# Kernel tuning notes

Hardware: AMD Instinct MI355X
Metric: run time of the kernel (lower is better)

## Reference

```python
import jax, jax.numpy as jnp
import numpy as np
import math

B, L, DM, DI, DS, DR, K, NL = 1, 1024, 768, 1536, 16, 48, 4, 2
DT_MIN, DT_MAX = 0.001, 0.1


def rmsnorm(x, w, eps=1e-5):
    return x * jax.lax.rsqrt(jnp.mean(x * x, axis=-1, keepdims=True) + eps) * w


def causal_dwconv(x, w, b):
    # x: [B,L,C], w: [C,1,K]. torch Conv1d(padding=K-1)[..., :L] == left-pad K-1 causal conv.
    y = jax.lax.conv_general_dilated(
        x.transpose(0, 2, 1), w, (1,), [(K - 1, 0)],
        dimension_numbers=('NCH', 'OIH', 'NCH'), feature_group_count=DI)
    return y.transpose(0, 2, 1) + b


def selective_scan(x, delta, A, Bm, Cm, D):
    # x, delta: [B,L,DI]; A: [DI,DS]; Bm, Cm: [B,L,DS]; D: [DI]
    dA = jnp.exp(delta[..., None] * A)               # [B,L,DI,DS]
    BX = (delta * x)[..., None] * Bm[:, :, None, :]  # [B,L,DI,DS]

    def comb(c1, c2):
        a1, b1 = c1
        a2, b2 = c2
        return (a1 * a2, a2 * b1 + b2)

    _, hs = jax.lax.associative_scan(comb, (dA, BX), axis=1)  # h_t = dA_t*h_{t-1} + BX_t
    return jnp.einsum('bldn,bln->bld', hs, Cm) + D * x


def ssm(x, xproj_w, dt_w, dt_b, A_log, D):
    dbc = jnp.einsum('bld,ed->ble', x, xproj_w)            # [B,L,DR+2*DS]
    dlt, Bm, Cm = jnp.split(dbc, [DR, DR + DS], axis=-1)
    delta = jax.nn.softplus(jnp.einsum('blr,dr->bld', dlt, dt_w) + dt_b)
    return selective_scan(x, delta, -jnp.exp(A_log), Bm, Cm, D)


def mamba_block(x, p):
    xz = jnp.einsum('bld,ed->ble', x, p['in_w'])           # [B,L,2*DI]
    xin, z = jnp.split(xz, 2, axis=-1)
    xf = jax.nn.silu(causal_dwconv(xin, p['cf_w'], p['cf_b']))
    xb = jax.nn.silu(causal_dwconv(xin[:, ::-1, :], p['cb_w'], p['cb_b']))
    yf = ssm(xf, p['xf_w'], p['dtf_w'], p['dtf_b'], p['Af'], p['Df'])
    yb = ssm(xb, p['xb_w'], p['dtb_w'], p['dtb_b'], p['Ab'], p['Db'])  # NOT flipped back (faithful)
    y = jnp.einsum('ble,de->bld', jnp.concatenate([yf, yb], axis=-1), p['pro_w']) + p['pro_b']
    # tokenizer: scores over L, softmax along L, mix values; dropout = identity (eval)
    att = jax.nn.softmax(jnp.einsum('bld,td->btl', y, p['wA']), axis=-1)  # [B,T=L,L]
    vv = jnp.einsum('bld,de->ble', y, p['wV'])
    y = jnp.einsum('btl,ble->bte', att, vv)
    return jnp.einsum('bld,od->blo', y * jax.nn.silu(z), p['out_w'])


def reference(x, norm_w, in_proj_w, conv_f_w, conv_f_b, conv_b_w, conv_b_b,
              xproj_f_w, xproj_b_w, dt_f_w, dt_f_b, dt_b_w, dt_b_b,
              A_log_f, D_f, A_log_b, D_b, out_w, token_wA, token_wV, pro_w, pro_b):
    for i in range(NL):
        p = dict(in_w=in_proj_w[i], cf_w=conv_f_w[i], cf_b=conv_f_b[i],
                 cb_w=conv_b_w[i], cb_b=conv_b_b[i], xf_w=xproj_f_w[i],
                 xb_w=xproj_b_w[i], dtf_w=dt_f_w[i], dtf_b=dt_f_b[i],
                 dtb_w=dt_b_w[i], dtb_b=dt_b_b[i], Af=A_log_f[i], Df=D_f[i],
                 Ab=A_log_b[i], Db=D_b[i], out_w=out_w[i], wA=token_wA[i],
                 wV=token_wV[i], pro_w=pro_w[i], pro_b=pro_b[i])
        x = x + mamba_block(rmsnorm(x, norm_w[i]), p)
    return x


def setup_inputs():
    key = jax.random.key(0)
    ks = jax.random.split(key, 16)
    rn = lambda k, sh, s=0.02: jax.random.normal(k, sh, jnp.float32) * s
    A_log = jnp.broadcast_to(jnp.log(jnp.arange(1, DS + 1, dtype=jnp.float32)), (NL, DI, DS))
    dt = jnp.exp(jax.random.uniform(ks[0], (NL, DI)) * (math.log(DT_MAX) - math.log(DT_MIN)) + math.log(DT_MIN))
    inv_dt = dt + jnp.log(-jnp.expm1(-dt))  # softplus^-1(dt)
    dt_std = DR ** -0.5
    kaiming = (2.0 / DI) ** 0.5
    return {
        'x': jax.random.normal(ks[1], (B, L, DM), jnp.float32),
        'norm_w': jnp.ones((NL, DM), jnp.float32),
        'in_proj_w': rn(ks[2], (NL, 2 * DI, DM)),
        'conv_f_w': rn(ks[3], (NL, DI, 1, K), 0.3),
        'conv_f_b': jnp.zeros((NL, DI), jnp.float32),
        'conv_b_w': rn(ks[4], (NL, DI, 1, K), 0.3),
        'conv_b_b': jnp.zeros((NL, DI), jnp.float32),
        'xproj_f_w': rn(ks[5], (NL, DR + 2 * DS, DI)),
        'xproj_b_w': rn(ks[6], (NL, DR + 2 * DS, DI)),
        'dt_f_w': jax.random.uniform(ks[7], (NL, DI, DR), jnp.float32, -dt_std, dt_std),
        'dt_f_b': inv_dt,
        'dt_b_w': jax.random.uniform(ks[8], (NL, DI, DR), jnp.float32, -dt_std, dt_std),
        'dt_b_b': inv_dt,
        'A_log_f': A_log,
        'D_f': jnp.ones((NL, DI), jnp.float32),
        'A_log_b': A_log,
        'D_b': jnp.ones((NL, DI), jnp.float32),
        'out_w': rn(ks[9], (NL, DM, DI)),
        'token_wA': rn(ks[10], (NL, L, DI), kaiming),
        'token_wV': rn(ks[11], (NL, DI, DI), kaiming),
        'pro_w': rn(ks[12], (NL, DI, 2 * DI)),
        'pro_b': jnp.zeros((NL, DI), jnp.float32),
    }
```

## Files before the change

### kernel.cpp

```cpp
#include <hip/hip_runtime.h>
#include <hip/hip_bf16.h>
#include <math.h>
#include <stdint.h>

#define LSEQ 1024
#define DMODEL 768
#define DINNER 1536
#define DSTATE 16
#define DRANK 48
#define KCONV 4
#define NLAYER 2
#define DBC 80
#define NQ 4
#define QL (LSEQ / NQ)
#define QCH (QL / 16)

typedef unsigned short u16;
typedef __attribute__((ext_vector_type(8))) __bf16 bf16x8;
typedef __attribute__((ext_vector_type(4))) float f32x4;
typedef __attribute__((ext_vector_type(4))) unsigned short us4;

__device__ __forceinline__ u16 f2bf(float f) {
  union { float f; unsigned u; } v; v.f = f;
  unsigned r = v.u + 0x7fffu + ((v.u >> 16) & 1u);
  return (u16)(r >> 16);
}
__device__ __forceinline__ float bf2f(u16 u) {
  union { unsigned u; float f; } v; v.u = ((unsigned)u) << 16;
  return v.f;
}

__device__ __forceinline__ void gload16(const void* g, void* l) {
  auto gp = reinterpret_cast<const __attribute__((address_space(1))) uint32_t*>(
      reinterpret_cast<uintptr_t>(g));
  auto lp = reinterpret_cast<__attribute__((address_space(3))) uint32_t*>(
      reinterpret_cast<uintptr_t>(l));
  __builtin_amdgcn_global_load_lds(gp, lp, 16, 0, 0);
}

#define CV0 589824
#define CV1 (CV0 + 1179648)
#define CV2 (CV1 + 393216)
#define CV3 (CV2 + 294912)
__global__ __launch_bounds__(256) void cvt4_k(
    const float* __restrict__ i0, u16* __restrict__ o0,
    const float* __restrict__ i1, u16* __restrict__ o1,
    const float* __restrict__ i2, u16* __restrict__ o2,
    const float* __restrict__ i3, u16* __restrict__ o3) {
  int i = blockIdx.x * 256 + threadIdx.x;
  const float* in; u16* out; int off;
  if (i < CV0)      { in = i0; out = o0; off = i; }
  else if (i < CV1) { in = i1; out = o1; off = i - CV0; }
  else if (i < CV2) { in = i2; out = o2; off = i - CV1; }
  else              { in = i3; out = o3; off = i - CV2; }
  float4 v = ((const float4*)in)[off];
  us4 o; o[0] = f2bf(v.x); o[1] = f2bf(v.y); o[2] = f2bf(v.z); o[3] = f2bf(v.w);
  ((us4*)out)[off] = o;
}

__global__ __launch_bounds__(256) void transcvt_k(const float* __restrict__ in,
                                                  u16* __restrict__ out,
                                                  int R, int C) {
  __shared__ float t[32][33];
  int c0 = blockIdx.x * 32, r0 = blockIdx.y * 32;
  int tx = threadIdx.x & 31, ty = threadIdx.x >> 5;
  for (int i = ty; i < 32; i += 8) t[i][tx] = in[(size_t)(r0 + i) * C + c0 + tx];
  __syncthreads();
  for (int i = ty; i < 32; i += 8)
    out[(size_t)(c0 + i) * R + r0 + tx] = f2bf(t[tx][i]);
}

__global__ __launch_bounds__(256) void transpose16_k(const u16* __restrict__ in,
                                                     u16* __restrict__ out,
                                                     int R, int C) {
  __shared__ u16 t[32][34];
  int c0 = blockIdx.x * 32, r0 = blockIdx.y * 32;
  int tx = threadIdx.x & 31, ty = threadIdx.x >> 5;
  for (int i = ty; i < 32; i += 8) t[i][tx] = in[(size_t)(r0 + i) * C + c0 + tx];
  __syncthreads();
  for (int i = ty; i < 32; i += 8)
    out[(size_t)(c0 + i) * R + r0 + tx] = t[tx][i];
}

__global__ __launch_bounds__(256) void rmsnorm_k(const float* __restrict__ x,
                                                 const float* __restrict__ w,
                                                 u16* __restrict__ xn) {
  int row = blockIdx.x;
  int tid = threadIdx.x;
  const float* xr = x + (size_t)row * DMODEL;
  float ss = 0.f;
  for (int j = tid; j < DMODEL; j += 256) { float v = xr[j]; ss += v * v; }
  __shared__ float red[256];
  red[tid] = ss; __syncthreads();
  for (int s = 128; s > 0; s >>= 1) { if (tid < s) red[tid] += red[tid + s]; __syncthreads(); }
  float scale = rsqrtf(red[0] / (float)DMODEL + 1e-5f);
  u16* outr = xn + (size_t)row * DMODEL;
  for (int j = tid; j < DMODEL; j += 256) outr[j] = f2bf(xr[j] * scale * w[j]);
}

template<int EPI>
__global__ __launch_bounds__(256) void mgemm_k(
    const u16* __restrict__ A, int lda,
    const u16* __restrict__ B, int ldb,
    void* __restrict__ Cv, int ldc, int K,
    const float* __restrict__ bias,
    const float* __restrict__ resid, int ldr)
{
  __shared__ u16 As[2][64 * 64];
  __shared__ u16 Bs[2][64 * 64];
  const int tid = threadIdx.x;
  const int lane = tid & 63;
  const int w = tid >> 6;

  const int nbx = gridDim.x;
  int bid = blockIdx.y * nbx + blockIdx.x;
  const int nwg = nbx * gridDim.y;
  bid = (bid & 7) * (nwg >> 3) + (bid >> 3);
  const int bm = (bid / nbx) * 64;
  const int bn = (bid % nbx) * 64;

  const int srow = lane >> 3;
  const int scs = (lane & 7) ^ srow;
  const int gA = 2 * w;
  const u16* Asrc0 = A + (size_t)(bm + gA * 8 + srow) * lda + scs * 8;
  const u16* Asrc1 = Asrc0 + (size_t)8 * lda;
  const u16* Bsrc0 = B + (size_t)(bn + gA * 8 + srow) * ldb + scs * 8;
  const u16* Bsrc1 = Bsrc0 + (size_t)8 * ldb;
  const int d0 = gA * 512;
  const int d1 = d0 + 512;

  const int fr = lane & 15;
  const int fs = lane >> 4;
  const int wm = (w >> 1) * 32;
  const int wn = (w & 1) * 32;
  int aoff[2][2], boff[2][2];
#pragma unroll
  for (int i = 0; i < 2; i++)
#pragma unroll
    for (int h = 0; h < 2; h++) {
      const int g = h * 4 + fs;
      aoff[i][h] = (wm + i * 16 + fr) * 64 + (g ^ (fr & 7)) * 8;
      boff[i][h] = (wn + i * 16 + fr) * 64 + (g ^ (fr & 7)) * 8;
    }

  f32x4 acc[2][2];
#pragma unroll
  for (int i = 0; i < 2; i++)
#pragma unroll
    for (int j = 0; j < 2; j++) acc[i][j] = (f32x4){0.f, 0.f, 0.f, 0.f};

#define STAGE(buf, k0) do { \
    gload16(Asrc0 + (k0), &As[buf][d0]); \
    gload16(Asrc1 + (k0), &As[buf][d1]); \
    gload16(Bsrc0 + (k0), &Bs[buf][d0]); \
    gload16(Bsrc1 + (k0), &Bs[buf][d1]); \
  } while (0)

  const int nk = K >> 6;
  STAGE(0, 0);

  for (int t = 0; t < nk; t++) {
    const int buf = t & 1;
    __syncthreads();
    if (t + 1 < nk) STAGE(buf ^ 1, (t + 1) << 6);
    const u16* As_ = As[buf];
    const u16* Bs_ = Bs[buf];
#pragma unroll
    for (int h = 0; h < 2; h++) {
      bf16x8 a0 = *reinterpret_cast<const bf16x8*>(As_ + aoff[0][h]);
      bf16x8 a1 = *reinterpret_cast<const bf16x8*>(As_ + aoff[1][h]);
      bf16x8 b0 = *reinterpret_cast<const bf16x8*>(Bs_ + boff[0][h]);
      bf16x8 b1 = *reinterpret_cast<const bf16x8*>(Bs_ + boff[1][h]);
      acc[0][0] = __builtin_amdgcn_mfma_f32_16x16x32_bf16(a0, b0, acc[0][0], 0, 0, 0);
      acc[0][1] = __builtin_amdgcn_mfma_f32_16x16x32_bf16(a0, b1, acc[0][1], 0, 0, 0);
      acc[1][0] = __builtin_amdgcn_mfma_f32_16x16x32_bf16(a1, b0, acc[1][0], 0, 0, 0);
      acc[1][1] = __builtin_amdgcn_mfma_f32_16x16x32_bf16(a1, b1, acc[1][1], 0, 0, 0);
    }
  }
#undef STAGE

#pragma unroll
  for (int i = 0; i < 2; i++) {
#pragma unroll
    for (int j = 0; j < 2; j++) {
      const int col = bn + wn + j * 16 + fr;
      const int row0 = bm + wm + i * 16 + fs * 4;
      float bv = (EPI & 1) ? bias[col] : 0.f;
#pragma unroll
      for (int r = 0; r < 4; r++) {
        float v = acc[i][j][r] + bv;
        if (EPI & 4) v += resid[(size_t)(row0 + r) * ldr + col];
        if (EPI & 16) {
          float z = resid[(size_t)(row0 + r) * ldr + col];
          v *= z / (1.f + __expf(-z));
        }
        if (EPI & 8) ((u16*)Cv)[(size_t)(row0 + r) * ldc + col] = f2bf(v);
        else         ((float*)Cv)[(size_t)(row0 + r) * ldc + col] = v;
      }
    }
  }
}

__global__ __launch_bounds__(256) void svgemm_k(
    const u16* __restrict__ wA, const u16* __restrict__ ypro,
    const u16* __restrict__ wVT,
    float* __restrict__ Smat, u16* __restrict__ vv)
{
  __shared__ u16 As[2][64 * 64];
  __shared__ u16 Bs[2][64 * 64];
  const int tid = threadIdx.x;
  const int lane = tid & 63;
  const int w = tid >> 6;

  int bid = blockIdx.x;
  bid = (bid & 7) * 80 + (bid >> 3);
  const bool is_s = bid < 256;
  const u16* A;
  const u16* B;
  int bm, bn;
  if (is_s) { A = wA;   B = ypro; bm = (bid >> 4) * 64;         bn = (bid & 15) * 64; }
  else      { A = ypro; B = wVT;  bm = ((bid - 256) / 24) * 64; bn = ((bid - 256) % 24) * 64; }

  const int srow = lane >> 3;
  const int scs = (lane & 7) ^ srow;
  const int gA = 2 * w;
  const u16* Asrc0 = A + (size_t)(bm + gA * 8 + srow) * DINNER + scs * 8;
  const u16* Asrc1 = Asrc0 + (size_t)8 * DINNER;
  const u16* Bsrc0 = B + (size_t)(bn + gA * 8 + srow) * DINNER + scs * 8;
  const u16* Bsrc1 = Bsrc0 + (size_t)8 * DINNER;
  const int d0 = gA * 512;
  const int d1 = d0 + 512;

  const int fr = lane & 15;
  const int fs = lane >> 4;
  const int wm = (w >> 1) * 32;
  const int wn = (w & 1) * 32;
  int aoff[2][2], boff[2][2];
#pragma unroll
  for (int i = 0; i < 2; i++)
#pragma unroll
    for (int h = 0; h < 2; h++) {
      const int g = h * 4 + fs;
      aoff[i][h] = (wm + i * 16 + fr) * 64 + (g ^ (fr & 7)) * 8;
      boff[i][h] = (wn + i * 16 + fr) * 64 + (g ^ (fr & 7)) * 8;
    }

  f32x4 acc[2][2];
#pragma unroll
  for (int i = 0; i < 2; i++)
#pragma unroll
    for (int j = 0; j < 2; j++) acc[i][j] = (f32x4){0.f, 0.f, 0.f, 0.f};

#define STAGE(buf, k0) do { \
    gload16(Asrc0 + (k0), &As[buf][d0]); \
    gload16(Asrc1 + (k0), &As[buf][d1]); \
    gload16(Bsrc0 + (k0), &Bs[buf][d0]); \
    gload16(Bsrc1 + (k0), &Bs[buf][d1]); \
  } while (0)

  STAGE(0, 0);
  for (int t = 0; t < DINNER / 64; t++) {
    const int buf = t & 1;
    __syncthreads();
    if (t + 1 < DINNER / 64) STAGE(buf ^ 1, (t + 1) << 6);
    const u16* As_ = As[buf];
    const u16* Bs_ = Bs[buf];
#pragma unroll
    for (int h = 0; h < 2; h++) {
      bf16x8 a0 = *reinterpret_cast<const bf16x8*>(As_ + aoff[0][h]);
      bf16x8 a1 = *reinterpret_cast<const bf16x8*>(As_ + aoff[1][h]);
      bf16x8 b0 = *reinterpret_cast<const bf16x8*>(Bs_ + boff[0][h]);
      bf16x8 b1 = *reinterpret_cast<const bf16x8*>(Bs_ + boff[1][h]);
      acc[0][0] = __builtin_amdgcn_mfma_f32_16x16x32_bf16(a0, b0, acc[0][0], 0, 0, 0);
      acc[0][1] = __builtin_amdgcn_mfma_f32_16x16x32_bf16(a0, b1, acc[0][1], 0, 0, 0);
      acc[1][0] = __builtin_amdgcn_mfma_f32_16x16x32_bf16(a1, b0, acc[1][0], 0, 0, 0);
      acc[1][1] = __builtin_amdgcn_mfma_f32_16x16x32_bf16(a1, b1, acc[1][1], 0, 0, 0);
    }
  }
#undef STAGE

#pragma unroll
  for (int i = 0; i < 2; i++) {
#pragma unroll
    for (int j = 0; j < 2; j++) {
      const int col = bn + wn + j * 16 + fr;
      const int row0 = bm + wm + i * 16 + fs * 4;
#pragma unroll
      for (int r = 0; r < 4; r++) {
        float v = acc[i][j][r];
        if (is_s) Smat[(size_t)(row0 + r) * LSEQ + col] = v;
        else      vv[(size_t)(row0 + r) * DINNER + col] = f2bf(v);
      }
    }
  }
}

#define TG_R 16
#define TG_KC 96
#define TG_KS 16

__global__ __launch_bounds__(256) void thin_gemm_k(
    const float* __restrict__ Af_, const float* __restrict__ Ab_,
    const float* __restrict__ Bf_, const float* __restrict__ Bb_,
    float* __restrict__ partial)
{
  __shared__ float As[TG_R][100];
  __shared__ float Bs[80][100];
  const float* A = blockIdx.z ? Ab_ : Af_;
  const float* B = blockIdx.z ? Bb_ : Bf_;
  float* part = partial + (size_t)blockIdx.z * TG_KS * LSEQ * DBC;
  const int tid = threadIdx.x;
  const int m0 = blockIdx.x * TG_R;
  const int ks = blockIdx.y;
  const int k0 = ks * TG_KC;

  for (int i = tid; i < 384; i += 256) {
    int r = i / 24, q = i % 24;
    *(float4*)&As[r][q * 4] = *(const float4*)(A + (size_t)(m0 + r) * DINNER + k0 + q * 4);
  }
  for (int i = tid; i < 1920; i += 256) {
    int r = i / 24, q = i % 24;
    *(float4*)&Bs[r][q * 4] = *(const float4*)(B + (size_t)r * DINNER + k0 + q * 4);
  }
  __syncthreads();

  const int r = tid >> 4;
  const int c0 = (tid & 15) * 5;
  float acc[5] = {};
  for (int k = 0; k < TG_KC; k++) {
    float a = As[r][k];
#pragma unroll
    for (int j = 0; j < 5; j++) acc[j] += a * Bs[c0 + j][k];
  }
  float* out = part + ((size_t)ks * LSEQ + m0 + r) * DBC + c0;
#pragma unroll
  for (int j = 0; j < 5; j++) out[j] = acc[j];
}

__global__ __launch_bounds__(256) void reduce_dbc_k(const float* __restrict__ partial,
                                                    float* __restrict__ outf,
                                                    float* __restrict__ outb) {
  int i = blockIdx.x * 256 + threadIdx.x;
  const float* part = partial + (size_t)blockIdx.y * TG_KS * LSEQ * DBC;
  float s = 0.f;
#pragma unroll
  for (int ks = 0; ks < TG_KS; ks++) s += part[(size_t)ks * (LSEQ * DBC) + i];
  (blockIdx.y ? outb : outf)[i] = s;
}

#define BM 64
#define BN 64
#define BK 16

__global__ __launch_bounds__(256) void delta_gemm_k(
    const float* __restrict__ A0, const float* __restrict__ A1,
    const float* __restrict__ B0, const float* __restrict__ B1,
    const float* __restrict__ b0, const float* __restrict__ b1,
    u16* __restrict__ C0, u16* __restrict__ C1)
{
  __shared__ float Asf[BK][BM];
  __shared__ float Bsf[BK][BN + 4];
  const float* A = blockIdx.z ? A1 : A0;
  const float* B = blockIdx.z ? B1 : B0;
  const float* bias = blockIdx.z ? b1 : b0;
  u16* C = blockIdx.z ? C1 : C0;
  const int tid = threadIdx.x;
  const int bm = blockIdx.y * BM;
  const int bn = blockIdx.x * BN;
  const int ar = tid >> 2;
  const int ak = (tid & 3) << 2;
  const int ty = tid >> 4, tx = tid & 15;
  float acc[4][4] = {};

  for (int k0 = 0; k0 < DRANK; k0 += BK) {
    float4 av = *(const float4*)(A + (size_t)(bm + ar) * DBC + k0 + ak);
    float4 bv = *(const float4*)(B + (size_t)(bn + ar) * DRANK + k0 + ak);
    __syncthreads();
    Asf[ak + 0][ar] = av.x; Asf[ak + 1][ar] = av.y;
    Asf[ak + 2][ar] = av.z; Asf[ak + 3][ar] = av.w;
    Bsf[ak + 0][ar] = bv.x; Bsf[ak + 1][ar] = bv.y;
    Bsf[ak + 2][ar] = bv.z; Bsf[ak + 3][ar] = bv.w;
    __syncthreads();
#pragma unroll
    for (int kk = 0; kk < BK; kk++) {
      float4 a4 = *(const float4*)&Asf[kk][ty * 4];
      float4 b4 = *(const float4*)&Bsf[kk][tx * 4];
      float a[4] = {a4.x, a4.y, a4.z, a4.w};
      float b[4] = {b4.x, b4.y, b4.z, b4.w};
#pragma unroll
      for (int i = 0; i < 4; i++)
#pragma unroll
        for (int j = 0; j < 4; j++)
          acc[i][j] += a[i] * b[j];
    }
  }

#pragma unroll
  for (int i = 0; i < 4; i++) {
    int row = bm + ty * 4 + i;
#pragma unroll
    for (int j = 0; j < 4; j++) {
      int col = bn + tx * 4 + j;
      float v = acc[i][j] + bias[col];
      v = (v > 20.f) ? v : log1pf(__expf(v));
      C[(size_t)row * DINNER + col] = f2bf(v);
    }
  }
}

__global__ __launch_bounds__(256) void conv_silu_k(
    const float* __restrict__ xz,
    const float* __restrict__ wf, const float* __restrict__ bf,
    const float* __restrict__ wb, const float* __restrict__ bb,
    float* __restrict__ xf, float* __restrict__ xb)
{
  int idx = blockIdx.x * 256 + threadIdx.x;
  int dir = blockIdx.y;
  if (idx >= LSEQ * DINNER) return;
  int l = idx / DINNER, c = idx % DINNER;
  const float* w = (dir ? wb : wf) + c * KCONV;
  float acc = (dir ? bb : bf)[c];
#pragma unroll
  for (int k = 0; k < KCONV; k++) {
    int ls = l - (KCONV - 1) + k;
    if (ls >= 0) {
      int lsrc = dir ? (LSEQ - 1 - ls) : ls;
      acc += w[k] * xz[(size_t)lsrc * (2 * DINNER) + c];
    }
  }
  float sv = acc / (1.f + __expf(-acc));
  (dir ? xb : xf)[idx] = sv;
}

__global__ __launch_bounds__(256) void scan_a_k(
    const float* __restrict__ xcf, const float* __restrict__ xcb,
    const u16* __restrict__ dltf, const u16* __restrict__ dltb,
    const float* __restrict__ dbcf, const float* __restrict__ dbcb,
    const float* __restrict__ Af, const float* __restrict__ Ab,
    float* __restrict__ qsP, float* __restrict__ qsQ)
{
  __shared__ float sP[16 * 16 * 16];
  __shared__ float sQ[16 * 16 * 16];
  const int dir = blockIdx.z;
  const int qid = blockIdx.y;
  const float* xc    = dir ? xcb : xcf;
  const u16*   delta = dir ? dltb : dltf;
  const float* dbc   = dir ? dbcb : dbcf;
  const float* A_log = dir ? Ab : Af;

  const int tid = threadIdx.x;
  const int c = tid >> 4;
  const int dl = tid & 15;
  const int d = blockIdx.x * 16 + dl;

  float Aa[DSTATE];
#pragma unroll
  for (int s = 0; s < DSTATE; s++) Aa[s] = -__expf(A_log[(size_t)d * DSTATE + s]);

  float aP[DSTATE], q[DSTATE];
#pragma unroll
  for (int s = 0; s < DSTATE; s++) { aP[s] = 1.f; q[s] = 0.f; }
  const int l0 = qid * QL + c * QCH;
  for (int i = 0; i < QCH; i++) {
    int l = l0 + i;
    float dt = bf2f(delta[(size_t)l * DINNER + d]);
    float dx = dt * xc[(size_t)l * DINNER + d];
    const float* bm = dbc + (size_t)l * DBC + DRANK;
#pragma unroll
    for (int s = 0; s < DSTATE; s++) {
      float a = __expf(dt * Aa[s]);
      q[s] = a * q[s] + dx * bm[s];
      aP[s] *= a;
    }
  }
#pragma unroll
  for (int s = 0; s < DSTATE; s++) {
    sP[(c * 16 + dl) * 16 + s] = aP[s];
    sQ[(c * 16 + dl) * 16 + s] = q[s];
  }
  __syncthreads();

  {
    const int d2 = tid >> 4, s2 = tid & 15;
    float h = 0.f, P = 1.f;
    for (int cc = 0; cc < 16; cc++) {
      int idx = (cc * 16 + d2) * 16 + s2;
      float a = sP[idx];
      h = a * h + sQ[idx];
      P *= a;
    }
    size_t o = (((size_t)dir * NQ + qid) * DINNER + blockIdx.x * 16 + d2) * 16 + s2;
    qsP[o] = P;
    qsQ[o] = h;
  }
}

__global__ __launch_bounds__(256) void scan_c_k(
    const float* __restrict__ xcf, const float* __restrict__ xcb,
    const u16* __restrict__ dltf, const u16* __restrict__ dltb,
    const float* __restrict__ dbcf, const float* __restrict__ dbcb,
    const float* __restrict__ Af, const float* __restrict__ Ab,
    const float* __restrict__ Df, const float* __restrict__ Db,
    const float* __restrict__ qsP, const float* __restrict__ qsQ,
    u16* __restrict__ ycat)
{
  __shared__ float sP[16 * 16 * 16];
  __shared__ float sQ[16 * 16 * 16];
  const int dir = blockIdx.z;
  const int qid = blockIdx.y;
  const float* xc    = dir ? xcb : xcf;
  const u16*   delta = dir ? dltb : dltf;
  const float* dbc   = dir ? dbcb : dbcf;
  const float* A_log = dir ? Ab : Af;
  const float* Dvec  = dir ? Db : Df;
  const int col_off  = dir ? DINNER : 0;

  const int tid = threadIdx.x;
  const int c = tid >> 4;
  const int dl = tid & 15;
  const int d = blockIdx.x * 16 + dl;

  float Aa[DSTATE];
#pragma unroll
  for (int s = 0; s < DSTATE; s++) Aa[s] = -__expf(A_log[(size_t)d * DSTATE + s]);

  float aP[DSTATE], q[DSTATE];
#pragma unroll
  for (int s = 0; s < DSTATE; s++) { aP[s] = 1.f; q[s] = 0.f; }
  const int l0 = qid * QL + c * QCH;
  for (int i = 0; i < QCH; i++) {
    int l = l0 + i;
    float dt = bf2f(delta[(size_t)l * DINNER + d]);
    float dx = dt * xc[(size_t)l * DINNER + d];
    const float* bm = dbc + (size_t)l * DBC + DRANK;
#pragma unroll
    for (int s = 0; s < DSTATE; s++) {
      float a = __expf(dt * Aa[s]);
      q[s] = a * q[s] + dx * bm[s];
      aP[s] *= a;
    }
  }
#pragma unroll
  for (int s = 0; s < DSTATE; s++) {
    sP[(c * 16 + dl) * 16 + s] = aP[s];
    sQ[(c * 16 + dl) * 16 + s] = q[s];
  }
  __syncthreads();

  {
    const int d2 = tid >> 4, s2 = tid & 15;
    size_t base = ((size_t)dir * NQ * DINNER + blockIdx.x * 16 + d2) * 16 + s2;
    float h = 0.f;
    for (int qq = 0; qq < qid; qq++) {
      size_t o = base + (size_t)qq * DINNER * 16;
      h = qsP[o] * h + qsQ[o];
    }
    for (int cc = 0; cc < 16; cc++) {
      int idx = (cc * 16 + d2) * 16 + s2;
      float a = sP[idx], qq = sQ[idx];
      sP[idx] = h;
      h = a * h + qq;
    }
  }
  __syncthreads();

  float hs[DSTATE];
#pragma unroll
  for (int s = 0; s < DSTATE; s++) hs[s] = sP[(c * 16 + dl) * 16 + s];
  const float Dd = Dvec[d];
  for (int i = 0; i < QCH; i++) {
    int l = l0 + i;
    float dt = bf2f(delta[(size_t)l * DINNER + d]);
    float xv = xc[(size_t)l * DINNER + d];
    float dx = dt * xv;
    const float* bm = dbc + (size_t)l * DBC + DRANK;
    const float* cm = bm + DSTATE;
    float y = 0.f;
#pragma unroll
    for (int s = 0; s < DSTATE; s++) {
      float a = __expf(dt * Aa[s]);
      hs[s] = a * hs[s] + dx * bm[s];
      y += hs[s] * cm[s];
    }
    ycat[(size_t)l * (2 * DINNER) + col_off + d] = f2bf(y + Dd * xv);
  }
}

__global__ __launch_bounds__(256) void softmax_k(const float* __restrict__ S,
                                                 u16* __restrict__ P) {
  int row = blockIdx.x, tid = threadIdx.x;
  __shared__ float buf[LSEQ];
  __shared__ float red[256];
  const float* r = S + (size_t)row * LSEQ;
  float m = -1e30f;
  for (int j = tid; j < LSEQ; j += 256) { float v = r[j]; buf[j] = v; m = fmaxf(m, v); }
  red[tid] = m; __syncthreads();
  for (int s = 128; s > 0; s >>= 1) { if (tid < s) red[tid] = fmaxf(red[tid], red[tid + s]); __syncthreads(); }
  m = red[0];
  __syncthreads();
  float sum = 0.f;
  for (int j = tid; j < LSEQ; j += 256) { float e = __expf(buf[j] - m); buf[j] = e; sum += e; }
  red[tid] = sum; __syncthreads();
  for (int s = 128; s > 0; s >>= 1) { if (tid < s) red[tid] += red[tid + s]; __syncthreads(); }
  float inv = 1.f / red[0];
  u16* pr = P + (size_t)row * LSEQ;
  for (int j = tid; j < LSEQ; j += 256) pr[j] = f2bf(buf[j] * inv);
}

extern "C" void kernel_launch(void* const* d_in, const int* in_sizes, int n_in,
                              void* d_out, int out_size, void* d_ws, size_t ws_size,
                              hipStream_t stream) {
  const float* in_x      = (const float*)d_in[0];
  const float* norm_w    = (const float*)d_in[1];
  const float* in_proj_w = (const float*)d_in[2];
  const float* conv_f_w  = (const float*)d_in[3];
  const float* conv_f_b  = (const float*)d_in[4];
  const float* conv_b_w  = (const float*)d_in[5];
  const float* conv_b_b  = (const float*)d_in[6];
  const float* xproj_f_w = (const float*)d_in[7];
  const float* xproj_b_w = (const float*)d_in[8];
  const float* dt_f_w    = (const float*)d_in[9];
  const float* dt_f_b    = (const float*)d_in[10];
  const float* dt_b_w    = (const float*)d_in[11];
  const float* dt_b_b    = (const float*)d_in[12];
  const float* A_log_f   = (const float*)d_in[13];
  const float* D_f       = (const float*)d_in[14];
  const float* A_log_b   = (const float*)d_in[15];
  const float* D_b       = (const float*)d_in[16];
  const float* out_w     = (const float*)d_in[17];
  const float* token_wA  = (const float*)d_in[18];
  const float* token_wV  = (const float*)d_in[19];
  const float* pro_w     = (const float*)d_in[20];
  const float* pro_b     = (const float*)d_in[21];

  float* ws = (float*)d_ws;
  float* xbuf = ws; ws += LSEQ * DMODEL;
  float* xz   = ws; ws += LSEQ * 2 * DINNER;
  float* xf   = ws; ws += LSEQ * DINNER;
  float* xb   = ws; ws += LSEQ * DINNER;
  float* dbcf = ws; ws += LSEQ * DBC;
  float* dbcb = ws; ws += LSEQ * DBC;
  float* delf_r = ws; ws += LSEQ * DINNER;
  float* delb_r = ws; ws += LSEQ * DINNER;
  float* scr  = ws; ws += LSEQ * DINNER;
  u16* xn_bf   = (u16*)ws; ws += (LSEQ * DMODEL) / 2;
  u16* ycat_bf = (u16*)ws; ws += LSEQ * DINNER;
  u16* ypro_bf = (u16*)ws; ws += (LSEQ * DINNER) / 2;
  u16* Wb      = (u16*)ws;
  u16* in_w_bf = Wb;
  u16* pw_bf   = in_w_bf + 3072 * 768;
  u16* wA_bf   = pw_bf + 1536 * 3072;
  u16* wVT_bf  = wA_bf + 1024 * 1536;
  u16* ow_bf   = wVT_bf + 1536 * 1536;

  float* dbc_part = delf_r;
  u16*   delf_bf  = (u16*)delf_r;
  u16*   delb_bf  = (u16*)delb_r;
  float* Smat     = delf_r;
  u16*   Smat_bf  = (u16*)delb_r;
  u16*   vv_bf    = (u16*)xf;
  u16*   vvT_bf   = (u16*)xb;
  u16*   g_bf     = ypro_bf;
  const int QS = 2 * NQ * DINNER * DSTATE;
  float* qsP   = scr;
  float* qsQ   = scr + QS;

  dim3 blk(256);
  for (int layer = 0; layer < NLAYER; layer++) {
    const float* nw  = norm_w    + (size_t)layer * DMODEL;
    const float* iw  = in_proj_w + (size_t)layer * 2 * DINNER * DMODEL;
    const float* cfw = conv_f_w  + (size_t)layer * DINNER * KCONV;
    const float* cfb = conv_f_b  + (size_t)layer * DINNER;
    const float* cbw = conv_b_w  + (size_t)layer * DINNER * KCONV;
    const float* cbb = conv_b_b  + (size_t)layer * DINNER;
    const float* xfw = xproj_f_w + (size_t)layer * DBC * DINNER;
    const float* xbw = xproj_b_w + (size_t)layer * DBC * DINNER;
    const float* dfw = dt_f_w    + (size_t)layer * DINNER * DRANK;
    const float* dfb = dt_f_b    + (size_t)layer * DINNER;
    const float* dbw = dt_b_w    + (size_t)layer * DINNER * DRANK;
    const float* dbb = dt_b_b    + (size_t)layer * DINNER;
    const float* Af  = A_log_f   + (size_t)layer * DINNER * DSTATE;
    const float* Df  = D_f       + (size_t)layer * DINNER;
    const float* Ab  = A_log_b   + (size_t)layer * DINNER * DSTATE;
    const float* Db  = D_b       + (size_t)layer * DINNER;
    const float* ow  = out_w     + (size_t)layer * DMODEL * DINNER;
    const float* wA  = token_wA  + (size_t)layer * LSEQ * DINNER;
    const float* wV  = token_wV  + (size_t)layer * DINNER * DINNER;
    const float* pw  = pro_w     + (size_t)layer * DINNER * 2 * DINNER;
    const float* pb  = pro_b     + (size_t)layer * DINNER;

    const float* xsrc = (layer == 0) ? in_x : xbuf;

    cvt4_k<<<CV3 / 256, blk, 0, stream>>>(iw, in_w_bf, pw, pw_bf, wA, wA_bf, ow, ow_bf);
    transcvt_k<<<dim3(1536 / 32, 1536 / 32), blk, 0, stream>>>(wV, wVT_bf, 1536, 1536);

    rmsnorm_k<<<LSEQ, blk, 0, stream>>>(xsrc, nw, xn_bf);

    mgemm_k<0><<<dim3(3072 / 64, LSEQ / 64), blk, 0, stream>>>(
        xn_bf, DMODEL, in_w_bf, DMODEL, xz, 2 * DINNER, DMODEL, nullptr, nullptr, 0);

    conv_silu_k<<<dim3((LSEQ * DINNER) / 256, 2), blk, 0, stream>>>(
        xz, cfw, cfb, cbw, cbb, xf, xb);

    thin_gemm_k<<<dim3(LSEQ / TG_R, TG_KS, 2), blk, 0, stream>>>(
        xf, xb, xfw, xbw, dbc_part);
    reduce_dbc_k<<<dim3((LSEQ * DBC) / 256, 2), blk, 0, stream>>>(
        dbc_part, dbcf, dbcb);

    delta_gemm_k<<<dim3(DINNER / BN, LSEQ / BM, 2), blk, 0, stream>>>(
        dbcf, dbcb, dfw, dbw, dfb, dbb, delf_bf, delb_bf);

    scan_a_k<<<dim3(DINNER / 16, NQ, 2), blk, 0, stream>>>(
        xf, xb, delf_bf, delb_bf, dbcf, dbcb, Af, Ab, qsP, qsQ);
    scan_c_k<<<dim3(DINNER / 16, NQ, 2), blk, 0, stream>>>(
        xf, xb, delf_bf, delb_bf, dbcf, dbcb, Af, Ab, Df, Db, qsP, qsQ, ycat_bf);

    mgemm_k<9><<<dim3(DINNER / 64, LSEQ / 64), blk, 0, stream>>>(
        ycat_bf, 2 * DINNER, pw_bf, 2 * DINNER, ypro_bf, DINNER, 2 * DINNER,
        pb, nullptr, 0);

    svgemm_k<<<640, blk, 0, stream>>>(wA_bf, ypro_bf, wVT_bf, Smat, vv_bf);
    softmax_k<<<LSEQ, blk, 0, stream>>>(Smat, Smat_bf);

    transpose16_k<<<dim3(DINNER / 32, LSEQ / 32), blk, 0, stream>>>(
        vv_bf, vvT_bf, LSEQ, DINNER);

    mgemm_k<24><<<dim3(DINNER / 64, LSEQ / 64), blk, 0, stream>>>(
        Smat_bf, LSEQ, vvT_bf, LSEQ, g_bf, DINNER, LSEQ,
        nullptr, xz + DINNER, 2 * DINNER);

    float* target = (layer == NLAYER - 1) ? (float*)d_out : xbuf;
    mgemm_k<4><<<dim3(DMODEL / 64, LSEQ / 64), blk, 0, stream>>>(
        g_bf, DINNER, ow_bf, DINNER, target, DMODEL, DINNER,
        nullptr, xsrc, DMODEL);
  }
}
```

Before: 423.5 us.

## Store xz and conv outputs in bf16 and widen scan parallelism

The in_proj GEMM now writes xz as bf16, and the conv/silu outputs xf/xb are stored as bf16. The thin GEMM, scan kernels and gating epilogue read these bf16 values, which halves memory traffic for these intermediates. The scan is also re-tiled to 8 sequence quarters, with 8 chunks of 32 channels per block, to raise parallelism and shorten the serial chunk loops. The cost is lower precision on the activations that feed the SSM, plus a longer cross-quarter prefix loop.

```diff
diff --git a/kernel.cpp b/kernel.cpp
--- a/kernel.cpp
+++ b/kernel.cpp
@@ -11,9 +11,11 @@
 #define KCONV 4
 #define NLAYER 2
 #define DBC 80
-#define NQ 4
+#define NQ 8
 #define QL (LSEQ / NQ)
-#define QCH (QL / 16)
+#define SCH 8
+#define SCW 32
+#define QCH (QL / SCH)
 
 typedef unsigned short u16;
 typedef __attribute__((ext_vector_type(8))) __bf16 bf16x8;
@@ -191,7 +193,9 @@
         float v = acc[i][j][r] + bv;
         if (EPI & 4) v += resid[(size_t)(row0 + r) * ldr + col];
         if (EPI & 16) {
-          float z = resid[(size_t)(row0 + r) * ldr + col];
+          float z = (EPI & 32)
+              ? bf2f(((const u16*)resid)[(size_t)(row0 + r) * ldr + col])
+              : resid[(size_t)(row0 + r) * ldr + col];
           v *= z / (1.f + __expf(-z));
         }
         if (EPI & 8) ((u16*)Cv)[(size_t)(row0 + r) * ldc + col] = f2bf(v);
@@ -300,13 +304,13 @@
 #define TG_KS 16
 
 __global__ __launch_bounds__(256) void thin_gemm_k(
-    const float* __restrict__ Af_, const float* __restrict__ Ab_,
+    const u16* __restrict__ Af_, const u16* __restrict__ Ab_,
     const float* __restrict__ Bf_, const float* __restrict__ Bb_,
     float* __restrict__ partial)
 {
-  __shared__ float As[TG_R][100];
+  __shared__ u16 As[TG_R][TG_KC];
   __shared__ float Bs[80][100];
-  const float* A = blockIdx.z ? Ab_ : Af_;
+  const u16* A = blockIdx.z ? Ab_ : Af_;
   const float* B = blockIdx.z ? Bb_ : Bf_;
   float* part = partial + (size_t)blockIdx.z * TG_KS * LSEQ * DBC;
   const int tid = threadIdx.x;
@@ -316,7 +320,7 @@
 
   for (int i = tid; i < 384; i += 256) {
     int r = i / 24, q = i % 24;
-    *(float4*)&As[r][q * 4] = *(const float4*)(A + (size_t)(m0 + r) * DINNER + k0 + q * 4);
+    *(us4*)&As[r][q * 4] = *(const us4*)(A + (size_t)(m0 + r) * DINNER + k0 + q * 4);
   }
   for (int i = tid; i < 1920; i += 256) {
     int r = i / 24, q = i % 24;
@@ -328,7 +332,7 @@
   const int c0 = (tid & 15) * 5;
   float acc[5] = {};
   for (int k = 0; k < TG_KC; k++) {
-    float a = As[r][k];
+    float a = bf2f(As[r][k]);
 #pragma unroll
     for (int j = 0; j < 5; j++) acc[j] += a * Bs[c0 + j][k];
   }
@@ -409,10 +413,10 @@
 }
 
 __global__ __launch_bounds__(256) void conv_silu_k(
-    const float* __restrict__ xz,
+    const u16* __restrict__ xz,
     const float* __restrict__ wf, const float* __restrict__ bf,
     const float* __restrict__ wb, const float* __restrict__ bb,
-    float* __restrict__ xf, float* __restrict__ xb)
+    u16* __restrict__ xf, u16* __restrict__ xb)
 {
   int idx = blockIdx.x * 256 + threadIdx.x;
   int dir = blockIdx.y;
@@ -425,33 +429,33 @@
     int ls = l - (KCONV - 1) + k;
     if (ls >= 0) {
       int lsrc = dir ? (LSEQ - 1 - ls) : ls;
-      acc += w[k] * xz[(size_t)lsrc * (2 * DINNER) + c];
+      acc += w[k] * bf2f(xz[(size_t)lsrc * (2 * DINNER) + c]);
     }
   }
   float sv = acc / (1.f + __expf(-acc));
-  (dir ? xb : xf)[idx] = sv;
+  (dir ? xb : xf)[idx] = f2bf(sv);
 }
 
 __global__ __launch_bounds__(256) void scan_a_k(
-    const float* __restrict__ xcf, const float* __restrict__ xcb,
+    const u16* __restrict__ xcf, const u16* __restrict__ xcb,
     const u16* __restrict__ dltf, const u16* __restrict__ dltb,
     const float* __restrict__ dbcf, const float* __restrict__ dbcb,
     const float* __restrict__ Af, const float* __restrict__ Ab,
     float* __restrict__ qsP, float* __restrict__ qsQ)
 {
-  __shared__ float sP[16 * 16 * 16];
-  __shared__ float sQ[16 * 16 * 16];
+  __shared__ float sP[SCH * SCW * DSTATE];
+  __shared__ float sQ[SCH * SCW * DSTATE];
   const int dir = blockIdx.z;
   const int qid = blockIdx.y;
-  const float* xc    = dir ? xcb : xcf;
+  const u16*   xc    = dir ? xcb : xcf;
   const u16*   delta = dir ? dltb : dltf;
   const float* dbc   = dir ? dbcb : dbcf;
   const float* A_log = dir ? Ab : Af;
 
   const int tid = threadIdx.x;
-  const int c = tid >> 4;
-  const int dl = tid & 15;
-  const int d = blockIdx.x * 16 + dl;
+  const int c = tid >> 5;
+  const int dl = tid & 31;
+  const int d = blockIdx.x * SCW + dl;
 
   float Aa[DSTATE];
 #pragma unroll
@@ -464,7 +468,7 @@
   for (int i = 0; i < QCH; i++) {
     int l = l0 + i;
     float dt = bf2f(delta[(size_t)l * DINNER + d]);
-    float dx = dt * xc[(size_t)l * DINNER + d];
+    float dx = dt * bf2f(xc[(size_t)l * DINNER + d]);
     const float* bm = dbc + (size_t)l * DBC + DRANK;
 #pragma unroll
     for (int s = 0; s < DSTATE; s++) {
@@ -475,28 +479,29 @@
   }
 #pragma unroll
   for (int s = 0; s < DSTATE; s++) {
-    sP[(c * 16 + dl) * 16 + s] = aP[s];
-    sQ[(c * 16 + dl) * 16 + s] = q[s];
+    sP[(c * SCW + dl) * DSTATE + s] = aP[s];
+    sQ[(c * SCW + dl) * DSTATE + s] = q[s];
   }
   __syncthreads();
 
-  {
-    const int d2 = tid >> 4, s2 = tid & 15;
+#pragma unroll
+  for (int pp = 0; pp < 2; pp++) {
+    const int p = tid + pp * 256;
+    const int d2 = p >> 4, s2 = p & 15;
     float h = 0.f, P = 1.f;
-    for (int cc = 0; cc < 16; cc++) {
-      int idx = (cc * 16 + d2) * 16 + s2;
-      float a = sP[idx];
-      h = a * h + sQ[idx];
-      P *= a;
-    }
-    size_t o = (((size_t)dir * NQ + qid) * DINNER + blockIdx.x * 16 + d2) * 16 + s2;
+    for (int cc = 0; cc < SCH; cc++) {
+      int idx = (cc * SCW + d2) * DSTATE + s2;
+      h = sP[idx] * h + sQ[idx];
+      P *= sP[idx];
+    }
+    size_t o = (((size_t)dir * NQ + qid) * DINNER + blockIdx.x * SCW + d2) * DSTATE + s2;
     qsP[o] = P;
     qsQ[o] = h;
   }
 }
 
 __global__ __launch_bounds__(256) void scan_c_k(
-    const float* __restrict__ xcf, const float* __restrict__ xcb,
+    const u16* __restrict__ xcf, const u16* __restrict__ xcb,
     const u16* __restrict__ dltf, const u16* __restrict__ dltb,
     const float* __restrict__ dbcf, const float* __restrict__ dbcb,
     const float* __restrict__ Af, const float* __restrict__ Ab,
@@ -504,11 +509,11 @@
     const float* __restrict__ qsP, const float* __restrict__ qsQ,
     u16* __restrict__ ycat)
 {
-  __shared__ float sP[16 * 16 * 16];
-  __shared__ float sQ[16 * 16 * 16];
+  __shared__ float sP[SCH * SCW * DSTATE];
+  __shared__ float sQ[SCH * SCW * DSTATE];
   const int dir = blockIdx.z;
   const int qid = blockIdx.y;
-  const float* xc    = dir ? xcb : xcf;
+  const u16*   xc    = dir ? xcb : xcf;
   const u16*   delta = dir ? dltb : dltf;
   const float* dbc   = dir ? dbcb : dbcf;
   const float* A_log = dir ? Ab : Af;
@@ -516,9 +521,9 @@
   const int col_off  = dir ? DINNER : 0;
 
   const int tid = threadIdx.x;
-  const int c = tid >> 4;
-  const int dl = tid & 15;
-  const int d = blockIdx.x * 16 + dl;
+  const int c = tid >> 5;
+  const int dl = tid & 31;
+  const int d = blockIdx.x * SCW + dl;
 
   float Aa[DSTATE];
 #pragma unroll
@@ -531,7 +536,7 @@
   for (int i = 0; i < QCH; i++) {
     int l = l0 + i;
     float dt = bf2f(delta[(size_t)l * DINNER + d]);
-    float dx = dt * xc[(size_t)l * DINNER + d];
+    float dx = dt * bf2f(xc[(size_t)l * DINNER + d]);
     const float* bm = dbc + (size_t)l * DBC + DRANK;
 #pragma unroll
     for (int s = 0; s < DSTATE; s++) {
@@ -542,36 +547,37 @@
   }
 #pragma unroll
   for (int s = 0; s < DSTATE; s++) {
-    sP[(c * 16 + dl) * 16 + s] = aP[s];
-    sQ[(c * 16 + dl) * 16 + s] = q[s];
+    sP[(c * SCW + dl) * DSTATE + s] = aP[s];
+    sQ[(c * SCW + dl) * DSTATE + s] = q[s];
   }
   __syncthreads();
 
-  {
-    const int d2 = tid >> 4, s2 = tid & 15;
-    size_t base = ((size_t)dir * NQ * DINNER + blockIdx.x * 16 + d2) * 16 + s2;
+#pragma unroll
+  for (int pp = 0; pp < 2; pp++) {
+    const int p = tid + pp * 256;
+    const int d2 = p >> 4, s2 = p & 15;
     float h = 0.f;
     for (int qq = 0; qq < qid; qq++) {
-      size_t o = base + (size_t)qq * DINNER * 16;
+      size_t o = (((size_t)dir * NQ + qq) * DINNER + blockIdx.x * SCW + d2) * DSTATE + s2;
       h = qsP[o] * h + qsQ[o];
     }
-    for (int cc = 0; cc < 16; cc++) {
-      int idx = (cc * 16 + d2) * 16 + s2;
-      float a = sP[idx], qq = sQ[idx];
+    for (int cc = 0; cc < SCH; cc++) {
+      int idx = (cc * SCW + d2) * DSTATE + s2;
+      float a = sP[idx], qv = sQ[idx];
       sP[idx] = h;
-      h = a * h + qq;
+      h = a * h + qv;
     }
   }
   __syncthreads();
 
   float hs[DSTATE];
 #pragma unroll
-  for (int s = 0; s < DSTATE; s++) hs[s] = sP[(c * 16 + dl) * 16 + s];
+  for (int s = 0; s < DSTATE; s++) hs[s] = sP[(c * SCW + dl) * DSTATE + s];
   const float Dd = Dvec[d];
   for (int i = 0; i < QCH; i++) {
     int l = l0 + i;
     float dt = bf2f(delta[(size_t)l * DINNER + d]);
-    float xv = xc[(size_t)l * DINNER + d];
+    float xv = bf2f(xc[(size_t)l * DINNER + d]);
     float dx = dt * xv;
     const float* bm = dbc + (size_t)l * DBC + DRANK;
     const float* cm = bm + DSTATE;
@@ -635,9 +641,9 @@
 
   float* ws = (float*)d_ws;
   float* xbuf = ws; ws += LSEQ * DMODEL;
-  float* xz   = ws; ws += LSEQ * 2 * DINNER;
-  float* xf   = ws; ws += LSEQ * DINNER;
-  float* xb   = ws; ws += LSEQ * DINNER;
+  u16* xz_bf  = (u16*)ws; ws += LSEQ * DINNER;
+  u16* xf_bf  = (u16*)ws; ws += (LSEQ * DINNER) / 2;
+  u16* xb_bf  = (u16*)ws; ws += (LSEQ * DINNER) / 2;
   float* dbcf = ws; ws += LSEQ * DBC;
   float* dbcb = ws; ws += LSEQ * DBC;
   float* delf_r = ws; ws += LSEQ * DINNER;
@@ -658,8 +664,8 @@
   u16*   delb_bf  = (u16*)delb_r;
   float* Smat     = delf_r;
   u16*   Smat_bf  = (u16*)delb_r;
-  u16*   vv_bf    = (u16*)xf;
-  u16*   vvT_bf   = (u16*)xb;
+  u16*   vv_bf    = xf_bf;
+  u16*   vvT_bf   = xb_bf;
   u16*   g_bf     = ypro_bf;
   const int QS = 2 * NQ * DINNER * DSTATE;
   float* qsP   = scr;
@@ -696,24 +702,24 @@
 
     rmsnorm_k<<<LSEQ, blk, 0, stream>>>(xsrc, nw, xn_bf);
 
-    mgemm_k<0><<<dim3(3072 / 64, LSEQ / 64), blk, 0, stream>>>(
-        xn_bf, DMODEL, in_w_bf, DMODEL, xz, 2 * DINNER, DMODEL, nullptr, nullptr, 0);
+    mgemm_k<8><<<dim3(3072 / 64, LSEQ / 64), blk, 0, stream>>>(
+        xn_bf, DMODEL, in_w_bf, DMODEL, xz_bf, 2 * DINNER, DMODEL, nullptr, nullptr, 0);
 
     conv_silu_k<<<dim3((LSEQ * DINNER) / 256, 2), blk, 0, stream>>>(
-        xz, cfw, cfb, cbw, cbb, xf, xb);
+        xz_bf, cfw, cfb, cbw, cbb, xf_bf, xb_bf);
 
     thin_gemm_k<<<dim3(LSEQ / TG_R, TG_KS, 2), blk, 0, stream>>>(
-        xf, xb, xfw, xbw, dbc_part);
+        xf_bf, xb_bf, xfw, xbw, dbc_part);
     reduce_dbc_k<<<dim3((LSEQ * DBC) / 256, 2), blk, 0, stream>>>(
         dbc_part, dbcf, dbcb);
 
     delta_gemm_k<<<dim3(DINNER / BN, LSEQ / BM, 2), blk, 0, stream>>>(
         dbcf, dbcb, dfw, dbw, dfb, dbb, delf_bf, delb_bf);
 
-    scan_a_k<<<dim3(DINNER / 16, NQ, 2), blk, 0, stream>>>(
-        xf, xb, delf_bf, delb_bf, dbcf, dbcb, Af, Ab, qsP, qsQ);
-    scan_c_k<<<dim3(DINNER / 16, NQ, 2), blk, 0, stream>>>(
-        xf, xb, delf_bf, delb_bf, dbcf, dbcb, Af, Ab, Df, Db, qsP, qsQ, ycat_bf);
+    scan_a_k<<<dim3(DINNER / SCW, NQ, 2), blk, 0, stream>>>(
+        xf_bf, xb_bf, delf_bf, delb_bf, dbcf, dbcb, Af, Ab, qsP, qsQ);
+    scan_c_k<<<dim3(DINNER / SCW, NQ, 2), blk, 0, stream>>>(
+        xf_bf, xb_bf, delf_bf, delb_bf, dbcf, dbcb, Af, Ab, Df, Db, qsP, qsQ, ycat_bf);
 
     mgemm_k<9><<<dim3(DINNER / 64, LSEQ / 64), blk, 0, stream>>>(
         ycat_bf, 2 * DINNER, pw_bf, 2 * DINNER, ypro_bf, DINNER, 2 * DINNER,
@@ -725,9 +731,9 @@
     transpose16_k<<<dim3(DINNER / 32, LSEQ / 32), blk, 0, stream>>>(
         vv_bf, vvT_bf, LSEQ, DINNER);
 
-    mgemm_k<24><<<dim3(DINNER / 64, LSEQ / 64), blk, 0, stream>>>(
+    mgemm_k<56><<<dim3(DINNER / 64, LSEQ / 64), blk, 0, stream>>>(
         Smat_bf, LSEQ, vvT_bf, LSEQ, g_bf, DINNER, LSEQ,
-        nullptr, xz + DINNER, 2 * DINNER);
+        nullptr, (const float*)(xz_bf + DINNER), 2 * DINNER);
 
     float* target = (layer == NLAYER - 1) ? (float*)d_out : xbuf;
     mgemm_k<4><<<dim3(DMODEL / 64, LSEQ / 64), blk, 0, stream>>>(
```

Result: faster. 413.8 us (-2.3%).
